# Optimization experiments

Hardware: AMD Instinct MI355X
Metric: run time of the kernel (lower is better)

The kernel has to match this reference:

```python
import jax, jax.numpy as jnp
import numpy as np

EPS = 1e-5   # torch BatchNorm2d default eps
HEADS = 4


def conv1x1_bn(x, w, g, b, m, v):
    # 1x1 conv (no bias) == channel matmul, then inference-mode BatchNorm
    y = jnp.einsum('oc,bchw->bohw', w, x)
    s = g / jnp.sqrt(v + EPS)
    return y * s[None, :, None, None] + (b - m * s)[None, :, None, None]


def dwconv3x3_bn(x, w, g, b, m, v):
    # depthwise 3x3 conv, padding 1 (autopad), groups=C, then BatchNorm
    C = x.shape[1]
    y = jax.lax.conv_general_dilated(
        x, w, window_strides=(1, 1), padding=((1, 1), (1, 1)),
        dimension_numbers=('NCHW', 'OIHW', 'NCHW'), feature_group_count=C)
    s = g / jnp.sqrt(v + EPS)
    return y * s[None, :, None, None] + (b - m * s)[None, :, None, None]


def split_heads(x):
    b, c, h, w = x.shape
    hd = c // HEADS
    return x.reshape(b, HEADS, hd, h * w).transpose(0, 1, 3, 2)  # [b,heads,n,hd]


def merge_heads(x, h, w):
    b, heads, n, hd = x.shape
    return x.transpose(0, 1, 3, 2).reshape(b, heads * hd, h, w)


def setup_inputs() -> dict:
    key = jax.random.key(0)
    B, C, H, W = 4, 256, 48, 48
    ks = jax.random.split(key, 32)
    inp = {
        'q': jax.random.normal(ks[0], (B, C, H, W), jnp.float32),
        'k': jax.random.normal(ks[1], (B, C, H, W), jnp.float32),
        'v': jax.random.normal(ks[2], (B, C, H, W), jnp.float32),
    }
    i = 3
    for name in ['wq', 'wk', 'wv', 'proj']:
        inp[name + '_w'] = jax.random.normal(ks[i], (C, C), jnp.float32) * 0.02; i += 1
    inp['pe_w'] = jax.random.normal(ks[i], (C, 1, 3, 3), jnp.float32) * 0.1; i += 1
    for name in ['wq', 'wk', 'wv', 'pe', 'proj']:
        inp[name + '_g'] = jax.random.uniform(ks[i], (C,), jnp.float32, 0.5, 1.5); i += 1
        inp[name + '_b'] = jax.random.normal(ks[i], (C,), jnp.float32) * 0.1; i += 1
        inp[name + '_m'] = jax.random.normal(ks[i], (C,), jnp.float32) * 0.1; i += 1
        inp[name + '_v'] = jax.random.uniform(ks[i], (C,), jnp.float32, 0.5, 1.5); i += 1
    return inp


def reference(q, k, v,
              wq_w, wk_w, wv_w, proj_w, pe_w,
              wq_g, wq_b, wq_m, wq_v,
              wk_g, wk_b, wk_m, wk_v,
              wv_g, wv_b, wv_m, wv_v,
              pe_g, pe_b, pe_m, pe_v,
              proj_g, proj_b, proj_m, proj_v):
    H, W = q.shape[2], q.shape[3]
    qf = conv1x1_bn(q, wq_w, wq_g, wq_b, wq_m, wq_v)
    kf = conv1x1_bn(k, wk_w, wk_g, wk_b, wk_m, wk_v)
    vf = conv1x1_bn(v, wv_w, wv_g, wv_b, wv_m, wv_v)
    qh = split_heads(qf)  # [b,heads,n,hd]
    kh = split_heads(kf)
    vh = split_heads(vf)
    scale = qh.shape[-1] ** -0.5
    attn = jax.nn.softmax(jnp.einsum('bhnd,bhmd->bhnm', qh, kh) * scale, axis=-1)
    y = jnp.einsum('bhnm,bhmd->bhnd', attn, vh)
    y = merge_heads(y, H, W) + dwconv3x3_bn(merge_heads(qh, H, W), pe_w, pe_g, pe_b, pe_m, pe_v)
    return conv1x1_bn(y, proj_w, proj_g, proj_b, proj_m, proj_v)
```

## Files before the change

### kernel.cpp

```cpp
#include <hip/hip_runtime.h>
#include <math.h>

#define HEADS 4
#define HD    64
#define CCH   256
#define NB    4
#define HH    48
#define WW    48
#define NN    (HH*WW)
#define EPSBN 1e-5f
#define KSCL  0.18033688f
#define BCN   (NB*CCH*NN)
#define NSP   4

typedef unsigned short ushort_t;
typedef __attribute__((ext_vector_type(8))) short bfrag;
typedef __attribute__((ext_vector_type(4))) float f32x4;

#define MFMA __builtin_amdgcn_mfma_f32_16x16x32_bf16

static __device__ __forceinline__ ushort_t f2bf(float x) {
    unsigned int u = __float_as_uint(x);
    unsigned int r = (u + 0x7fffu + ((u >> 16) & 1u)) >> 16;
    return (ushort_t)r;
}
static __device__ __forceinline__ unsigned cvtpk(float lo, float hi) {
    unsigned r;
    asm("v_cvt_pk_bf16_f32 %0, %1, %2" : "=v"(r) : "v"(lo), "v"(hi));
    return r;
}
static __device__ __forceinline__ float bflo(unsigned u) { return __uint_as_float(u << 16); }
static __device__ __forceinline__ float bfhi(unsigned u) { return __uint_as_float(u & 0xffff0000u); }

static __device__ __forceinline__ void gload16(const void* g, void* l) {
    __builtin_amdgcn_global_load_lds(
        (const __attribute__((address_space(1))) void*)g,
        (__attribute__((address_space(3))) void*)l, 16, 0, 0);
}

__global__ __launch_bounds__(256)
void prep_transpose(const float* __restrict__ q, const float* __restrict__ k,
                    const float* __restrict__ v, ushort_t* __restrict__ Xt)
{
    const int blk = blockIdx.x;
    const int t  = blk / 1152;
    const int r  = blk % 1152;
    const int b  = r / 288;
    const int r2 = r % 288;
    const int n0 = (r2 >> 3) * 64;
    const int cb = (r2 & 7) * 32;
    const float* X = (t == 0) ? q : (t == 1) ? k : v;
    ushort_t* O = Xt + (size_t)t * BCN;
    const int lane = threadIdx.x & 63;
    const int c0   = cb + (threadIdx.x >> 6) * 8;
    const float* src = X + ((size_t)(b * CCH + c0) * NN + n0 + lane);
    float vv[8];
#pragma unroll
    for (int j = 0; j < 8; ++j) vv[j] = src[(size_t)j * NN];
    uint4 u;
    u.x = cvtpk(vv[0], vv[1]); u.y = cvtpk(vv[2], vv[3]);
    u.z = cvtpk(vv[4], vv[5]); u.w = cvtpk(vv[6], vv[7]);
    *(uint4*)&O[((size_t)b * NN + n0 + lane) * CCH + c0] = u;
}

struct PrepWP {
    const float* W[4];
    const float* G[4]; const float* Bb[4]; const float* Mm[4]; const float* Vv[4];
    const float* pew; const float* peg; const float* peb; const float* pem; const float* pev;
    ushort_t* W4; float* bias4; ushort_t* pw2; float* pbias; float* kmax2;
};
__global__ __launch_bounds__(256)
void prep_w(PrepWP P)
{
    const int blk = blockIdx.x, tid = threadIdx.x;
    if (blk == 128) {
        int c = tid;
        float s = P.peg[c] * rsqrtf(P.pev[c] + EPSBN);
        for (int tap = 0; tap < 9; ++tap)
            P.pw2[tap * CCH + c] = f2bf(P.pew[c * 9 + tap] * s);
        P.pbias[c] = P.peb[c] - P.pem[c] * s;
        if (tid < 16) P.kmax2[tid] = 0.f;
        return;
    }
    int g  = blk * 256 + tid;
    int cv = g >> 13;
    int o  = (g >> 5) & 255;
    int c8 = g & 31;
    float s  = P.G[cv][o] * rsqrtf(P.Vv[cv][o] + EPSBN);
    float s2 = (cv == 1) ? s * KSCL : s;
    const float* w = P.W[cv] + (size_t)o * CCH + c8 * 8;
    uint4 u;
    u.x = cvtpk(w[0]*s2, w[1]*s2); u.y = cvtpk(w[2]*s2, w[3]*s2);
    u.z = cvtpk(w[4]*s2, w[5]*s2); u.w = cvtpk(w[6]*s2, w[7]*s2);
    *(uint4*)&P.W4[((size_t)cv * CCH + o) * CCH + c8 * 8] = u;
    if (c8 == 0) {
        float bb = (P.Bb[cv][o] - P.Mm[cv][o] * s);
        P.bias4[cv * CCH + o] = (cv == 1) ? bb * KSCL : bb;
    }
}

template<int PROJ>
__global__ __launch_bounds__(256)
void conv_gemm(const ushort_t* __restrict__ T, const ushort_t* __restrict__ W4,
               const float* __restrict__ bias4,
               ushort_t* __restrict__ qnd, ushort_t* __restrict__ knd,
               ushort_t* __restrict__ vcn, float* __restrict__ outf,
               float* __restrict__ kmax2)
{
    __shared__ ushort_t Ts[64][264];
    __shared__ ushort_t Ws[64][264];
    const int nt = blockIdx.x, ot = blockIdx.y, z = blockIdx.z;
    const int which = PROJ ? 3 : (z >> 2);
    const int b = z & 3;
    const int tid = threadIdx.x;
    const int n0 = nt * 64, o0 = ot * 64;
    const ushort_t* Tsrc = T + (PROJ ? (size_t)0 : (size_t)which * BCN) + ((size_t)b * NN + n0) * CCH;
    const ushort_t* Wsrc = W4 + (size_t)which * CCH * CCH + (size_t)o0 * CCH;
    const float*    bias = bias4 + which * CCH;
#pragma unroll
    for (int i = 0; i < 8; ++i) {
        int idx = tid + i * 256;
        int r = idx >> 5, c16 = idx & 31;
        *(uint4*)&Ts[r][c16 * 8] = *(const uint4*)&Tsrc[(size_t)r * CCH + c16 * 8];
        *(uint4*)&Ws[r][c16 * 8] = *(const uint4*)&Wsrc[(size_t)r * CCH + c16 * 8];
    }
    __syncthreads();
    const int wv = tid >> 6, lane = tid & 63, lr = lane & 15, lg = lane >> 4;
    const int qn = (wv >> 1) * 32, qo = (wv & 1) * 32;
    f32x4 acc[2][2];
#pragma unroll
    for (int i = 0; i < 2; ++i)
#pragma unroll
        for (int j = 0; j < 2; ++j) acc[i][j] = (f32x4){0.f, 0.f, 0.f, 0.f};

    if (!PROJ && (z >> 2) < 2) {
#pragma unroll
        for (int k8 = 0; k8 < 8; ++k8) {
            const int kc = k8 * 32 + lg * 8;
            bfrag ta0 = *(const bfrag*)&Ts[qn + lr][kc];
            bfrag ta1 = *(const bfrag*)&Ts[qn + 16 + lr][kc];
            bfrag wa0 = *(const bfrag*)&Ws[qo + lr][kc];
            bfrag wa1 = *(const bfrag*)&Ws[qo + 16 + lr][kc];
            acc[0][0] = MFMA(ta0, wa0, acc[0][0], 0, 0, 0);
            acc[0][1] = MFMA(ta0, wa1, acc[0][1], 0, 0, 0);
            acc[1][0] = MFMA(ta1, wa0, acc[1][0], 0, 0, 0);
            acc[1][1] = MFMA(ta1, wa1, acc[1][1], 0, 0, 0);
        }
    } else {
#pragma unroll
        for (int k8 = 0; k8 < 8; ++k8) {
            const int kc = k8 * 32 + lg * 8;
            bfrag ta0 = *(const bfrag*)&Ts[qn + lr][kc];
            bfrag ta1 = *(const bfrag*)&Ts[qn + 16 + lr][kc];
            bfrag wa0 = *(const bfrag*)&Ws[qo + lr][kc];
            bfrag wa1 = *(const bfrag*)&Ws[qo + 16 + lr][kc];
            acc[0][0] = MFMA(wa0, ta0, acc[0][0], 0, 0, 0);
            acc[0][1] = MFMA(wa0, ta1, acc[0][1], 0, 0, 0);
            acc[1][0] = MFMA(wa1, ta0, acc[1][0], 0, 0, 0);
            acc[1][1] = MFMA(wa1, ta1, acc[1][1], 0, 0, 0);
        }
    }

    __syncthreads();
    if (!PROJ && which < 2) {
        ushort_t (*Ot)[72] = (ushort_t(*)[72])Ts;
        float bv[2] = { bias[o0 + qo + lr], bias[o0 + qo + 16 + lr] };
#pragma unroll
        for (int i = 0; i < 2; ++i)
#pragma unroll
            for (int j = 0; j < 2; ++j)
#pragma unroll
                for (int r = 0; r < 4; ++r)
                    Ot[qn + i * 16 + lg * 4 + r][qo + j * 16 + lr] = f2bf(acc[i][j][r] + bv[j]);
        __syncthreads();
        ushort_t* out = (which == 0) ? qnd : knd;
        for (int idx = tid; idx < 512; idx += 256) {
            int r = idx >> 3, sg = idx & 7;
            *(uint4*)&out[(((size_t)b * HEADS + ot) * NN + n0 + r) * HD + sg * 8] =
                *(const uint4*)&Ot[r][sg * 8];
        }
        if (which == 1 && tid < 64) {
            float s = 0.f;
#pragma unroll
            for (int j = 0; j < 8; ++j) {
                uint4 u = *(const uint4*)&Ot[tid][j * 8];
                s += bflo(u.x)*bflo(u.x) + bfhi(u.x)*bfhi(u.x);
                s += bflo(u.y)*bflo(u.y) + bfhi(u.y)*bfhi(u.y);
                s += bflo(u.z)*bflo(u.z) + bfhi(u.z)*bfhi(u.z);
                s += bflo(u.w)*bflo(u.w) + bfhi(u.w)*bfhi(u.w);
            }
            atomicMax((unsigned*)&kmax2[b * HEADS + ot], __float_as_uint(s));
        }
    } else if (!PROJ) {
        ushort_t (*Ot)[72] = (ushort_t(*)[72])Ts;
#pragma unroll
        for (int i = 0; i < 2; ++i)
#pragma unroll
            for (int r = 0; r < 4; ++r) {
                float bv = bias[o0 + qo + i * 16 + lg * 4 + r];
#pragma unroll
                for (int j = 0; j < 2; ++j)
                    Ot[qo + i * 16 + lg * 4 + r][qn + j * 16 + lr] = f2bf(acc[i][j][r] + bv);
            }
        __syncthreads();
        for (int idx = tid; idx < 512; idx += 256) {
            int r = idx >> 3, sg = idx & 7;
            *(uint4*)&vcn[((size_t)b * CCH + o0 + r) * NN + n0 + sg * 8] =
                *(const uint4*)&Ot[r][sg * 8];
        }
    } else {
        float (*Of)[68] = (float(*)[68])Ts;
#pragma unroll
        for (int i = 0; i < 2; ++i)
#pragma unroll
            for (int r = 0; r < 4; ++r) {
                float bv = bias[o0 + qo + i * 16 + lg * 4 + r];
#pragma unroll
                for (int j = 0; j < 2; ++j)
                    Of[qo + i * 16 + lg * 4 + r][qn + j * 16 + lr] = acc[i][j][r] + bv;
            }
        __syncthreads();
        for (int idx = tid; idx < 1024; idx += 256) {
            int r = idx >> 4, c4 = idx & 15;
            *(float4*)&outf[((size_t)b * CCH + o0 + r) * NN + n0 + c4 * 4] =
                *(const float4*)&Of[r][c4 * 4];
        }
    }
}

__global__ __launch_bounds__(256, 4)
void attn_kernel(const ushort_t* __restrict__ Qnd,
                 const ushort_t* __restrict__ Knd,
                 const ushort_t* __restrict__ Vcn,
                 const float* __restrict__ kmax2,
                 ushort_t* __restrict__ Op,
                 float* __restrict__ Larr)
{
    __shared__ __align__(16) char smem[40960];

    const int tid = threadIdx.x;
    const int lin0 = blockIdx.x + 18 * blockIdx.y + 288 * blockIdx.z;
    const int w    = (lin0 & 7) * 144 + (lin0 >> 3);
    const int qt = w % 18;
    const int bh = (w / 18) & 15;
    const int sp = w / 288;
    const int b = bh >> 2, h = bh & 3;
    const int lane = tid & 63, wv = tid >> 6;
    const int lr = lane & 15, lg = lane >> 4;
    const int lrow = lane >> 3, lslot = (lane & 7) ^ lrow;
    const int n0 = qt * 128;
    const size_t ndb = (size_t)(b * HEADS + h) * NN * HD;
    const size_t cnb = ((size_t)b * CCH + h * HD) * NN;

    const char* kgp = (const char*)(Knd + ndb) + (size_t)(sp * 576 + wv * 16 + lrow) * 128 + lslot * 16;
    const char* vgp = (const char*)(Vcn + cnb + sp * 576) + (size_t)(wv * 16 + lrow) * (NN * 2) + lslot * 16;
    char* kls = smem + wv * 2048;
    char* vls = smem + 16384 + wv * 2048;

#define STAGE(buf, t) do { \
    const char* kp_ = kgp + (size_t)(t) * 8192; \
    const char* vp_ = vgp + (size_t)(t) * 128; \
    char* kd_ = kls + (buf) * 8192; \
    char* vd_ = vls + (buf) * 8192; \
    gload16(kp_,               kd_); \
    gload16(kp_ + 1024,        kd_ + 1024); \
    gload16(vp_,               vd_); \
    gload16(vp_ + 8 * (NN*2),  vd_ + 1024); \
} while (0)

    bfrag qb[2][2];
    {
        const ushort_t* qbase = Qnd + ndb + (size_t)(n0 + wv * 32 + lr) * HD;
        qb[0][0] = *(const bfrag*)&qbase[lg * 8];
        qb[0][1] = *(const bfrag*)&qbase[32 + lg * 8];
        qb[1][0] = *(const bfrag*)&qbase[16 * HD + lg * 8];
        qb[1][1] = *(const bfrag*)&qbase[16 * HD + 32 + lg * 8];
    }
    float m0[2];
    {
        const float kmx = sqrtf(kmax2[bh]);
#pragma unroll
        for (int qc = 0; qc < 2; ++qc) {
            const unsigned* u0 = (const unsigned*)&qb[qc][0];
            const unsigned* u1 = (const unsigned*)&qb[qc][1];
            float s = 0.f;
#pragma unroll
            for (int j = 0; j < 4; ++j) {
                float a0 = bflo(u0[j]), a1 = bfhi(u0[j]);
                float b0 = bflo(u1[j]), b1 = bfhi(u1[j]);
                s += a0*a0 + a1*a1 + b0*b0 + b1*b1;
            }
            s += __shfl_xor(s, 16);
            s += __shfl_xor(s, 32);
            m0[qc] = sqrtf(s) * kmx + 0.5f;
        }
    }
    bfrag ones_f;
    {
        short ov = (lr == 0) ? (short)0x3F80 : (short)0;
#pragma unroll
        for (int j = 0; j < 8; ++j) ones_f[j] = ov;
    }

    f32x4 o[2][4], o4[2];
#pragma unroll
    for (int qc = 0; qc < 2; ++qc) {
        o4[qc] = (f32x4){0.f, 0.f, 0.f, 0.f};
#pragma unroll
        for (int db = 0; db < 4; ++db) o[qc][db] = (f32x4){0.f, 0.f, 0.f, 0.f};
    }

    char* Pw = smem + 32768 + wv * 2048;
    const int sw0 = (lg ^ (lr & 7)) << 4;
    const int sw1 = ((4 + lg) ^ (lr & 7)) << 4;

    STAGE(0, 0);
    __syncthreads();

    for (int t = 0; t < 9; ++t) {
        const int cur = t & 1;
        if (t < 8) STAGE(cur ^ 1, t + 1);
        const char* Kb = smem + cur * 8192;
        const char* Vb = smem + 16384 + cur * 8192;

        f32x4 st[2][4];
#pragma unroll
        for (int kb = 0; kb < 4; ++kb) {
            const char* krow = Kb + (kb * 16 + lr) * 128;
            bfrag ka0 = *(const bfrag*)(krow + sw0);
            bfrag ka1 = *(const bfrag*)(krow + sw1);
            f32x4 z0 = (f32x4){-m0[0], -m0[0], -m0[0], -m0[0]};
            z0 = MFMA(ka0, qb[0][0], z0, 0, 0, 0);
            st[0][kb] = MFMA(ka1, qb[0][1], z0, 0, 0, 0);
            f32x4 z1 = (f32x4){-m0[1], -m0[1], -m0[1], -m0[1]};
            z1 = MFMA(ka0, qb[1][0], z1, 0, 0, 0);
            st[1][kb] = MFMA(ka1, qb[1][1], z1, 0, 0, 0);
        }

        bfrag pb[2][2];
#pragma unroll
        for (int qc = 0; qc < 2; ++qc) {
            char* prow = Pw + lr * 128;
#pragma unroll
            for (int kb = 0; kb < 4; ++kb) {
                float p0 = exp2f(st[qc][kb][0]);
                float p1 = exp2f(st[qc][kb][1]);
                float p2 = exp2f(st[qc][kb][2]);
                float p3 = exp2f(st[qc][kb][3]);
                uint2 u; u.x = cvtpk(p0, p1); u.y = cvtpk(p2, p3);
                int slot = (2 * kb + (lg >> 1)) ^ (lr & 7);
                *(uint2*)(prow + slot * 16 + (lg & 1) * 8) = u;
            }
            pb[qc][0] = *(const bfrag*)(prow + sw0);
            pb[qc][1] = *(const bfrag*)(prow + sw1);
        }

#pragma unroll
        for (int db = 0; db < 4; ++db) {
            const char* vrow = Vb + (db * 16 + lr) * 128;
            bfrag va0 = *(const bfrag*)(vrow + sw0);
            bfrag va1 = *(const bfrag*)(vrow + sw1);
            o[0][db] = MFMA(va0, pb[0][0], o[0][db], 0, 0, 0);
            o[0][db] = MFMA(va1, pb[0][1], o[0][db], 0, 0, 0);
            o[1][db] = MFMA(va0, pb[1][0], o[1][db], 0, 0, 0);
            o[1][db] = MFMA(va1, pb[1][1], o[1][db], 0, 0, 0);
        }
        o4[0] = MFMA(ones_f, pb[0][0], o4[0], 0, 0, 0);
        o4[0] = MFMA(ones_f, pb[0][1], o4[0], 0, 0, 0);
        o4[1] = MFMA(ones_f, pb[1][0], o4[1], 0, 0, 0);
        o4[1] = MFMA(ones_f, pb[1][1], o4[1], 0, 0, 0);

        __syncthreads();
    }
#undef STAGE

    if (lg == 0) {
#pragma unroll
        for (int qc = 0; qc < 2; ++qc)
            Larr[(size_t)(sp * 16 + bh) * NN + n0 + wv * 32 + qc * 16 + lr] = o4[qc][0];
    }
    unsigned (*Osb)[36] = (unsigned(*)[36])smem;
#pragma unroll
    for (int qc = 0; qc < 2; ++qc) {
        int row = wv * 32 + qc * 16 + lr;
#pragma unroll
        for (int db = 0; db < 4; ++db) {
            Osb[row][db * 8 + lg * 2 + 0] = cvtpk(o[qc][db][0], o[qc][db][1]);
            Osb[row][db * 8 + lg * 2 + 1] = cvtpk(o[qc][db][2], o[qc][db][3]);
        }
    }
    __syncthreads();
    ushort_t* opb = Op + (size_t)sp * BCN + ((size_t)b * NN + n0) * CCH + h * HD;
    for (int idx = tid; idx < 1024; idx += 256) {
        int n = idx >> 3, s4 = idx & 7;
        *(uint4*)&opb[(size_t)n * CCH + s4 * 8] = *(const uint4*)&Osb[n][s4 * 4];
    }
}

__global__ __launch_bounds__(256)
void fuse_kernel(const ushort_t* __restrict__ Op, const float* __restrict__ Larr,
                 const ushort_t* __restrict__ Qnd,
                 const ushort_t* __restrict__ pw2, const float* __restrict__ pbias,
                 ushort_t* __restrict__ yt)
{
    const int tid = threadIdx.x;
    const int b  = blockIdx.x / 288;
    const int n0 = (blockIdx.x % 288) * 8;
    const int c8 = tid & 31, ns = tid >> 5;
    const int n  = n0 + ns;
    const int h  = c8 >> 3, c0 = c8 * 8;

    const ushort_t* o0p = Op + ((size_t)b * NN + n) * CCH + c0;
    float acc[8] = {0.f, 0.f, 0.f, 0.f, 0.f, 0.f, 0.f, 0.f};
#pragma unroll
    for (int s = 0; s < NSP; ++s) {
        uint4 u = *(const uint4*)&o0p[(size_t)s * BCN];
        acc[0] += bflo(u.x); acc[1] += bfhi(u.x);
        acc[2] += bflo(u.y); acc[3] += bfhi(u.y);
        acc[4] += bflo(u.z); acc[5] += bfhi(u.z);
        acc[6] += bflo(u.w); acc[7] += bfhi(u.w);
    }
    int mi = (b * HEADS + h) * NN + n;
    float ls = 0.f;
#pragma unroll
    for (int s = 0; s < NSP; ++s) ls += Larr[(size_t)s * 16 * NN + mi];
    float rinv = 1.0f / ls;
#pragma unroll
    for (int j = 0; j < 8; ++j) acc[j] *= rinv;

    const int x = n % WW, y = n / WW;
    const ushort_t* qb = Qnd + (size_t)(b * HEADS + h) * NN * HD + (c8 & 7) * 8;
#pragma unroll
    for (int ky = 0; ky < 3; ++ky) {
        int yy = y + ky - 1;
        if (yy < 0 || yy >= HH) continue;
#pragma unroll
        for (int kx = 0; kx < 3; ++kx) {
            int xx = x + kx - 1;
            if (xx < 0 || xx >= WW) continue;
            int np = yy * WW + xx;
            uint4 qv = *(const uint4*)&qb[(size_t)np * HD];
            uint4 w4 = *(const uint4*)&pw2[(ky * 3 + kx) * CCH + c0];
            acc[0] += bflo(qv.x) * bflo(w4.x); acc[1] += bfhi(qv.x) * bfhi(w4.x);
            acc[2] += bflo(qv.y) * bflo(w4.y); acc[3] += bfhi(qv.y) * bfhi(w4.y);
            acc[4] += bflo(qv.z) * bflo(w4.z); acc[5] += bfhi(qv.z) * bfhi(w4.z);
            acc[6] += bflo(qv.w) * bflo(w4.w); acc[7] += bfhi(qv.w) * bfhi(w4.w);
        }
    }
    float4 p0 = *(const float4*)&pbias[c0];
    float4 p1 = *(const float4*)&pbias[c0 + 4];
    acc[0] += p0.x; acc[1] += p0.y; acc[2] += p0.z; acc[3] += p0.w;
    acc[4] += p1.x; acc[5] += p1.y; acc[6] += p1.z; acc[7] += p1.w;
    uint4 u;
    u.x = cvtpk(acc[0], acc[1]); u.y = cvtpk(acc[2], acc[3]);
    u.z = cvtpk(acc[4], acc[5]); u.w = cvtpk(acc[6], acc[7]);
    *(uint4*)&yt[((size_t)b * NN + n) * CCH + c0] = u;
}

extern "C" void kernel_launch(void* const* d_in, const int* in_sizes, int n_in,
                              void* d_out, int out_size, void* d_ws, size_t ws_size,
                              hipStream_t stream) {
    const float* q = (const float*)d_in[0];
    const float* k = (const float*)d_in[1];
    const float* v = (const float*)d_in[2];

    char* ws = (char*)d_ws;
    ushort_t* qnd  = (ushort_t*)(ws + 0);
    ushort_t* knd  = (ushort_t*)(ws + 4718592);
    ushort_t* vcn  = (ushort_t*)(ws + 9437184);
    ushort_t* Xt   = (ushort_t*)(ws + 14155776);
    ushort_t* Op   = (ushort_t*)(ws + 14155776);
    ushort_t* yt   = (ushort_t*)(ws + 4718592);
    float*    Larr = (float*)   (ws + 33030144);
    ushort_t* W4   = (ushort_t*)(ws + 33619968);
    float*    bias4= (float*)   (ws + 34144256);
    ushort_t* pw2  = (ushort_t*)(ws + 34148352);
    float*    pbias= (float*)   (ws + 34152960);
    float*    kmax2= (float*)   (ws + 34156032);

    prep_transpose<<<3456, 256, 0, stream>>>(q, k, v, Xt);

    PrepWP P;
    P.W[0] = (const float*)d_in[3]; P.W[1] = (const float*)d_in[4];
    P.W[2] = (const float*)d_in[5]; P.W[3] = (const float*)d_in[6];
    P.G[0]  = (const float*)d_in[8];  P.Bb[0] = (const float*)d_in[9];
    P.Mm[0] = (const float*)d_in[10]; P.Vv[0] = (const float*)d_in[11];
    P.G[1]  = (const float*)d_in[12]; P.Bb[1] = (const float*)d_in[13];
    P.Mm[1] = (const float*)d_in[14]; P.Vv[1] = (const float*)d_in[15];
    P.G[2]  = (const float*)d_in[16]; P.Bb[2] = (const float*)d_in[17];
    P.Mm[2] = (const float*)d_in[18]; P.Vv[2] = (const float*)d_in[19];
    P.G[3]  = (const float*)d_in[24]; P.Bb[3] = (const float*)d_in[25];
    P.Mm[3] = (const float*)d_in[26]; P.Vv[3] = (const float*)d_in[27];
    P.pew = (const float*)d_in[7];
    P.peg = (const float*)d_in[20]; P.peb = (const float*)d_in[21];
    P.pem = (const float*)d_in[22]; P.pev = (const float*)d_in[23];
    P.W4 = W4; P.bias4 = bias4; P.pw2 = pw2; P.pbias = pbias; P.kmax2 = kmax2;
    prep_w<<<129, 256, 0, stream>>>(P);

    conv_gemm<0><<<dim3(36, 4, 12), 256, 0, stream>>>(Xt, W4, bias4, qnd, knd, vcn, nullptr, kmax2);

    attn_kernel<<<dim3(18, 16, NSP), 256, 0, stream>>>(qnd, knd, vcn, kmax2, Op, Larr);

    fuse_kernel<<<1152, 256, 0, stream>>>(Op, Larr, qnd, pw2, pbias, yt);

    conv_gemm<1><<<dim3(36, 4, 4), 256, 0, stream>>>(yt, W4, bias4, nullptr, nullptr, nullptr,
                                                     (float*)d_out, nullptr);
}
```

Baseline: 93.77 us.

## Merge prep kernels and reuse V double-buffer slot for P tile in attention

Folds the input transpose and weight-prep kernels into a single launch to save one kernel launch. In the attention kernel, the softmax probabilities are now written to the idle half of the V double buffer instead of a dedicated LDS region, which cuts shared memory from 40 KB to 32 KB. The next V tile's prefetch is delayed until after the P fragments have been read back. Exponentials are computed right after each QK MFMA. Delaying the V prefetch shortens the overlap window for V loads, in exchange for lower LDS use and possibly higher occupancy.

```diff
diff --git a/kernel.cpp b/kernel.cpp
--- a/kernel.cpp
+++ b/kernel.cpp
@@ -38,42 +38,40 @@
         (__attribute__((address_space(3))) void*)l, 16, 0, 0);
 }
 
-__global__ __launch_bounds__(256)
-void prep_transpose(const float* __restrict__ q, const float* __restrict__ k,
-                    const float* __restrict__ v, ushort_t* __restrict__ Xt)
-{
-    const int blk = blockIdx.x;
-    const int t  = blk / 1152;
-    const int r  = blk % 1152;
-    const int b  = r / 288;
-    const int r2 = r % 288;
-    const int n0 = (r2 >> 3) * 64;
-    const int cb = (r2 & 7) * 32;
-    const float* X = (t == 0) ? q : (t == 1) ? k : v;
-    ushort_t* O = Xt + (size_t)t * BCN;
-    const int lane = threadIdx.x & 63;
-    const int c0   = cb + (threadIdx.x >> 6) * 8;
-    const float* src = X + ((size_t)(b * CCH + c0) * NN + n0 + lane);
-    float vv[8];
-#pragma unroll
-    for (int j = 0; j < 8; ++j) vv[j] = src[(size_t)j * NN];
-    uint4 u;
-    u.x = cvtpk(vv[0], vv[1]); u.y = cvtpk(vv[2], vv[3]);
-    u.z = cvtpk(vv[4], vv[5]); u.w = cvtpk(vv[6], vv[7]);
-    *(uint4*)&O[((size_t)b * NN + n0 + lane) * CCH + c0] = u;
-}
-
 struct PrepWP {
     const float* W[4];
     const float* G[4]; const float* Bb[4]; const float* Mm[4]; const float* Vv[4];
     const float* pew; const float* peg; const float* peb; const float* pem; const float* pev;
     ushort_t* W4; float* bias4; ushort_t* pw2; float* pbias; float* kmax2;
+    const float* q; const float* k; const float* v; ushort_t* Xt;
 };
 __global__ __launch_bounds__(256)
-void prep_w(PrepWP P)
+void prep_kernel(PrepWP P)
 {
     const int blk = blockIdx.x, tid = threadIdx.x;
-    if (blk == 128) {
+    if (blk < 3456) {
+        const int t  = blk / 1152;
+        const int r  = blk % 1152;
+        const int b  = r / 288;
+        const int r2 = r % 288;
+        const int n0 = (r2 >> 3) * 64;
+        const int cb = (r2 & 7) * 32;
+        const float* X = (t == 0) ? P.q : (t == 1) ? P.k : P.v;
+        ushort_t* O = P.Xt + (size_t)t * BCN;
+        const int lane = tid & 63;
+        const int c0   = cb + (tid >> 6) * 8;
+        const float* src = X + ((size_t)(b * CCH + c0) * NN + n0 + lane);
+        float vv[8];
+#pragma unroll
+        for (int j = 0; j < 8; ++j) vv[j] = src[(size_t)j * NN];
+        uint4 u;
+        u.x = cvtpk(vv[0], vv[1]); u.y = cvtpk(vv[2], vv[3]);
+        u.z = cvtpk(vv[4], vv[5]); u.w = cvtpk(vv[6], vv[7]);
+        *(uint4*)&O[((size_t)b * NN + n0 + lane) * CCH + c0] = u;
+        return;
+    }
+    const int wb = blk - 3456;
+    if (wb == 128) {
         int c = tid;
         float s = P.peg[c] * rsqrtf(P.pev[c] + EPSBN);
         for (int tap = 0; tap < 9; ++tap)
@@ -82,7 +80,7 @@
         if (tid < 16) P.kmax2[tid] = 0.f;
         return;
     }
-    int g  = blk * 256 + tid;
+    int g  = wb * 256 + tid;
     int cv = g >> 13;
     int o  = (g >> 5) & 255;
     int c8 = g & 31;
@@ -236,7 +234,7 @@
                  ushort_t* __restrict__ Op,
                  float* __restrict__ Larr)
 {
-    __shared__ __align__(16) char smem[40960];
+    __shared__ __align__(16) char smem[32768];
 
     const int tid = threadIdx.x;
     const int lin0 = blockIdx.x + 18 * blockIdx.y + 288 * blockIdx.z;
@@ -257,15 +255,17 @@
     char* kls = smem + wv * 2048;
     char* vls = smem + 16384 + wv * 2048;
 
-#define STAGE(buf, t) do { \
+#define STAGE_K(buf, t) do { \
     const char* kp_ = kgp + (size_t)(t) * 8192; \
+    char* kd_ = kls + (buf) * 8192; \
+    gload16(kp_,        kd_); \
+    gload16(kp_ + 1024, kd_ + 1024); \
+} while (0)
+#define STAGE_V(buf, t) do { \
     const char* vp_ = vgp + (size_t)(t) * 128; \
-    char* kd_ = kls + (buf) * 8192; \
     char* vd_ = vls + (buf) * 8192; \
-    gload16(kp_,               kd_); \
-    gload16(kp_ + 1024,        kd_ + 1024); \
-    gload16(vp_,               vd_); \
-    gload16(vp_ + 8 * (NN*2),  vd_ + 1024); \
+    gload16(vp_,              vd_); \
+    gload16(vp_ + 8 * (NN*2), vd_ + 1024); \
 } while (0)
 
     bfrag qb[2][2];
@@ -310,20 +310,21 @@
         for (int db = 0; db < 4; ++db) o[qc][db] = (f32x4){0.f, 0.f, 0.f, 0.f};
     }
 
-    char* Pw = smem + 32768 + wv * 2048;
     const int sw0 = (lg ^ (lr & 7)) << 4;
     const int sw1 = ((4 + lg) ^ (lr & 7)) << 4;
 
-    STAGE(0, 0);
+    STAGE_K(0, 0);
+    STAGE_V(0, 0);
     __syncthreads();
 
     for (int t = 0; t < 9; ++t) {
         const int cur = t & 1;
-        if (t < 8) STAGE(cur ^ 1, t + 1);
+        if (t < 8) STAGE_K(cur ^ 1, t + 1);
         const char* Kb = smem + cur * 8192;
         const char* Vb = smem + 16384 + cur * 8192;
-
-        f32x4 st[2][4];
+        char* Pw = smem + 16384 + (cur ^ 1) * 8192 + wv * 2048;
+
+        uint2 pd[2][4];
 #pragma unroll
         for (int kb = 0; kb < 4; ++kb) {
             const char* krow = Kb + (kb * 16 + lr) * 128;
@@ -331,10 +332,14 @@
             bfrag ka1 = *(const bfrag*)(krow + sw1);
             f32x4 z0 = (f32x4){-m0[0], -m0[0], -m0[0], -m0[0]};
             z0 = MFMA(ka0, qb[0][0], z0, 0, 0, 0);
-            st[0][kb] = MFMA(ka1, qb[0][1], z0, 0, 0, 0);
+            f32x4 s0 = MFMA(ka1, qb[0][1], z0, 0, 0, 0);
             f32x4 z1 = (f32x4){-m0[1], -m0[1], -m0[1], -m0[1]};
             z1 = MFMA(ka0, qb[1][0], z1, 0, 0, 0);
-            st[1][kb] = MFMA(ka1, qb[1][1], z1, 0, 0, 0);
+            f32x4 s1 = MFMA(ka1, qb[1][1], z1, 0, 0, 0);
+            pd[0][kb].x = cvtpk(exp2f(s0[0]), exp2f(s0[1]));
+            pd[0][kb].y = cvtpk(exp2f(s0[2]), exp2f(s0[3]));
+            pd[1][kb].x = cvtpk(exp2f(s1[0]), exp2f(s1[1]));
+            pd[1][kb].y = cvtpk(exp2f(s1[2]), exp2f(s1[3]));
         }
 
         bfrag pb[2][2];
@@ -343,17 +348,14 @@
             char* prow = Pw + lr * 128;
 #pragma unroll
             for (int kb = 0; kb < 4; ++kb) {
-                float p0 = exp2f(st[qc][kb][0]);
-                float p1 = exp2f(st[qc][kb][1]);
-                float p2 = exp2f(st[qc][kb][2]);
-                float p3 = exp2f(st[qc][kb][3]);
-                uint2 u; u.x = cvtpk(p0, p1); u.y = cvtpk(p2, p3);
                 int slot = (2 * kb + (lg >> 1)) ^ (lr & 7);
-                *(uint2*)(prow + slot * 16 + (lg & 1) * 8) = u;
+                *(uint2*)(prow + slot * 16 + (lg & 1) * 8) = pd[qc][kb];
             }
             pb[qc][0] = *(const bfrag*)(prow + sw0);
             pb[qc][1] = *(const bfrag*)(prow + sw1);
         }
+        asm volatile("s_waitcnt lgkmcnt(0)" ::: "memory");
+        if (t < 8) STAGE_V(cur ^ 1, t + 1);
 
 #pragma unroll
         for (int db = 0; db < 4; ++db) {
@@ -372,7 +374,8 @@
 
         __syncthreads();
     }
-#undef STAGE
+#undef STAGE_K
+#undef STAGE_V
 
     if (lg == 0) {
 #pragma unroll
@@ -460,10 +463,6 @@
 extern "C" void kernel_launch(void* const* d_in, const int* in_sizes, int n_in,
                               void* d_out, int out_size, void* d_ws, size_t ws_size,
                               hipStream_t stream) {
-    const float* q = (const float*)d_in[0];
-    const float* k = (const float*)d_in[1];
-    const float* v = (const float*)d_in[2];
-
     char* ws = (char*)d_ws;
     ushort_t* qnd  = (ushort_t*)(ws + 0);
     ushort_t* knd  = (ushort_t*)(ws + 4718592);
@@ -477,8 +476,6 @@
     ushort_t* pw2  = (ushort_t*)(ws + 34148352);
     float*    pbias= (float*)   (ws + 34152960);
     float*    kmax2= (float*)   (ws + 34156032);
-
-    prep_transpose<<<3456, 256, 0, stream>>>(q, k, v, Xt);
 
     PrepWP P;
     P.W[0] = (const float*)d_in[3]; P.W[1] = (const float*)d_in[4];
@@ -495,7 +492,10 @@
     P.peg = (const float*)d_in[20]; P.peb = (const float*)d_in[21];
     P.pem = (const float*)d_in[22]; P.pev = (const float*)d_in[23];
     P.W4 = W4; P.bias4 = bias4; P.pw2 = pw2; P.pbias = pbias; P.kmax2 = kmax2;
-    prep_w<<<129, 256, 0, stream>>>(P);
+    P.q = (const float*)d_in[0]; P.k = (const float*)d_in[1];
+    P.v = (const float*)d_in[2]; P.Xt = Xt;
+
+    prep_kernel<<<3585, 256, 0, stream>>>(P);
 
     conv_gemm<0><<<dim3(36, 4, 12), 256, 0, stream>>>(Xt, W4, bias4, qnd, knd, vcn, nullptr, kmax2);
 
```

Measured after the change: 93.64 us. About the same (-0.1%).
